# Optimization experiments

Hardware: AMD Instinct MI355X
Metric: run time of the kernel (lower is better)

Reference implementation:

```python
import jax, jax.numpy as jnp
import numpy as np

N_NODES, N_EDGES, D_FEAT, D_HID, K_CHEB = 30000, 480000, 256, 256, 2


def setup_inputs() -> dict:
    N, E, D, H, K = N_NODES, N_EDGES, D_FEAT, D_HID, K_CHEB
    key = jax.random.key(0)
    ks = jax.random.split(key, 24)
    sD = 1.0 / np.sqrt(D)
    sH = 1.0 / np.sqrt(H)
    inp = {
        "x": jax.random.normal(ks[0], (N, D), jnp.float32),
        "edge_index": jax.random.randint(ks[1], (2, E), 0, N),
        "edge_weight": jax.random.uniform(ks[2], (E,), jnp.float32),
        "h": jax.random.normal(ks[3], (N, H), jnp.float32),
        "c": jax.random.normal(ks[4], (N, H), jnp.float32),
        "src_neighbor_ids": jax.random.randint(ks[5], (E,), 0, N),
        "dst_neighbor_ids": jax.random.randint(ks[6], (E,), 0, N),
    }
    for j, nm in enumerate(["W_i", "W_f", "W_g", "W_o"]):
        inp[nm] = jax.random.normal(ks[7 + j], (D, H), jnp.float32) * sD
    for j, nm in enumerate(["Wc_i", "Wc_f", "Wc_g", "Wc_o"]):
        inp[nm] = jax.random.normal(ks[11 + j], (K, H, H), jnp.float32) * sH
    for nm in ["bc_i", "bc_f", "bc_g", "bc_o", "b_i", "b_f", "b_g", "b_o", "b_lin"]:
        inp[nm] = jnp.zeros((H,), jnp.float32)
    for j, nm in enumerate(["w_ci", "w_cf", "w_co"]):
        inp[nm] = jax.random.normal(ks[15 + j], (H,), jnp.float32) * 0.1
    inp["W_lin"] = jax.random.normal(ks[18], (H, H), jnp.float32) * sH
    return inp


def _cheb_conv(h, src, dst, norm, W, b):
    # ChebConv, K=2, sym norm, lambda_max=2: T0 = h, T1 = L_hat h = -D^-1/2 A D^-1/2 h
    out = h @ W[0]
    t1 = jax.ops.segment_sum(norm[:, None] * h[src], dst, num_segments=h.shape[0])
    return out + t1 @ W[1] + b


def reference(x, edge_index, edge_weight, h, c, src_neighbor_ids, dst_neighbor_ids,
              W_i, W_f, W_g, W_o, Wc_i, Wc_f, Wc_g, Wc_o,
              bc_i, bc_f, bc_g, bc_o, w_ci, w_cf, w_co,
              b_i, b_f, b_g, b_o, W_lin, b_lin):
    src, dst = edge_index[0], edge_index[1]
    n = x.shape[0]
    # neighbor-feature augmentation: gather both BEFORE any update, then scatter-add
    snf = x[src_neighbor_ids]
    dnf = x[dst_neighbor_ids]
    x = x.at[src].add(snf)
    x = x.at[dst].add(dnf)
    # symmetric Chebyshev normalization (lambda_max = 2 -> diagonal of L_hat is 0)
    deg = jax.ops.segment_sum(edge_weight, src, num_segments=n)
    dinv = jnp.where(deg > 0, jax.lax.rsqrt(jnp.maximum(deg, 1e-12)), 0.0)
    norm = -dinv[src] * edge_weight * dinv[dst]
    # GCLSTM gates
    i = jax.nn.sigmoid(x @ W_i + _cheb_conv(h, src, dst, norm, Wc_i, bc_i) + w_ci * c + b_i)
    f = jax.nn.sigmoid(x @ W_f + _cheb_conv(h, src, dst, norm, Wc_f, bc_f) + w_cf * c + b_f)
    g = jnp.tanh(x @ W_g + _cheb_conv(h, src, dst, norm, Wc_g, bc_g) + b_g)
    c_new = f * c + i * g
    o = jax.nn.sigmoid(x @ W_o + _cheb_conv(h, src, dst, norm, Wc_o, bc_o) + w_co * c_new + b_o)
    h0 = o * jnp.tanh(c_new)
    h_out = jax.nn.relu(h0) @ W_lin + b_lin
    return (h_out, h0, c_new)
```

## Files before the change

kernel.cpp:

```cpp
#include <hip/hip_runtime.h>
#include <math.h>

#define NN 30000
#define NE 480000
#define DH 256
#define NH (NN * DH)
#define MPAD 30080
#define CAP 48

typedef _Float16 f16x2 __attribute__((ext_vector_type(2)));
typedef _Float16 f16x4 __attribute__((ext_vector_type(4)));
typedef _Float16 f16x8 __attribute__((ext_vector_type(8)));
typedef float f32x4 __attribute__((ext_vector_type(4)));

static __device__ __forceinline__ float sigmoidf_(float x) {
    return 1.0f / (1.0f + __expf(-x));
}
static __device__ __forceinline__ float tanhf_(float x) {
    return 1.0f - 2.0f / (1.0f + __expf(2.0f * x));
}
static __device__ __forceinline__ float rsq_(float d) {
    return (d > 0.0f) ? rsqrtf(fmaxf(d, 1e-12f)) : 0.0f;
}

static __device__ __forceinline__ unsigned char f16_to_f8(_Float16 hf) {
    unsigned short b = __builtin_bit_cast(unsigned short, hf);
    unsigned s = (b >> 15) & 1u, e = (b >> 10) & 31u, m = b & 1023u;
    int ne = (int)e - 8;
    unsigned m3 = (m + 64u) >> 7;
    if (m3 == 8u) { m3 = 0u; ne += 1; }
    if (ne <= 0) return (unsigned char)(s << 7);
    if (ne > 15) ne = 15;
    return (unsigned char)((s << 7) | ((unsigned)ne << 3) | m3);
}

static __device__ __forceinline__ void f8x4_to_f32s(unsigned g, float* o) {
    unsigned m4 = g & 0x7f7f7f7fu;
    unsigned s4 = g & 0x80808080u;
#if __has_builtin(__builtin_amdgcn_perm)
    unsigned mlo = __builtin_amdgcn_perm(0u, m4, 0x04010400u);
    unsigned mhi = __builtin_amdgcn_perm(0u, m4, 0x04030402u);
    unsigned slo = __builtin_amdgcn_perm(0u, s4, 0x04010400u);
    unsigned shi = __builtin_amdgcn_perm(0u, s4, 0x04030402u);
    unsigned lo = (mlo << 7) | (slo << 8);
    unsigned hi = (mhi << 7) | (shi << 8);
#else
    unsigned lo = ((m4 & 0xffu) << 7) | ((m4 & 0xff00u) << 15)
                | ((s4 & 0xffu) << 8) | ((s4 & 0xff00u) << 16);
    unsigned hi = (((m4 >> 16) & 0xffu) << 7) | ((m4 >> 16) & 0xff00u) << 15
                | (((s4 >> 16) & 0xffu) << 8) | (((s4 >> 16) & 0xff00u) << 16);
#endif
    f16x2 vlo = __builtin_bit_cast(f16x2, lo);
    f16x2 vhi = __builtin_bit_cast(f16x2, hi);
    o[0] = (float)vlo[0]; o[1] = (float)vlo[1];
    o[2] = (float)vhi[0]; o[3] = (float)vhi[1];
}

static __device__ __forceinline__ void gload16(const _Float16* g, _Float16* l) {
    __builtin_amdgcn_global_load_lds(
        (const __attribute__((address_space(1))) void*)g,
        (__attribute__((address_space(3))) void*)l, 16, 0, 0);
}


__global__ void deg_kernel(const int* __restrict__ src, const float* __restrict__ ew,
                           float* __restrict__ deg) {
    int e = blockIdx.x * blockDim.x + threadIdx.x;
    if (e < NE) atomicAdd(&deg[src[e]], ew[e]);
}


__global__ void mega1(const int* __restrict__ src, const int* __restrict__ dst,
                      const int* __restrict__ snf, const int* __restrict__ dnf,
                      const float* __restrict__ ew,
                      int* __restrict__ cntS, int* __restrict__ cntD,
                      int* __restrict__ slotS, int2* __restrict__ slotD,
                      const float* __restrict__ x, _Float16* __restrict__ x16,
                      const float* __restrict__ h, _Float16* __restrict__ h16,
                      unsigned char* __restrict__ h8,
                      const float* __restrict__ W_i, const float* __restrict__ W_f,
                      const float* __restrict__ W_g, const float* __restrict__ W_o,
                      const float* __restrict__ Wc_i, const float* __restrict__ Wc_f,
                      const float* __restrict__ Wc_g, const float* __restrict__ Wc_o,
                      const float* __restrict__ W_lin,
                      const float* __restrict__ bc_i, const float* __restrict__ bc_f,
                      const float* __restrict__ bc_g, const float* __restrict__ bc_o,
                      const float* __restrict__ b_i, const float* __restrict__ b_f,
                      const float* __restrict__ b_g, const float* __restrict__ b_o,
                      const float* __restrict__ w_ci, const float* __restrict__ w_cf,
                      const float* __restrict__ w_co,
                      _Float16* __restrict__ WcatT, _Float16* __restrict__ WlinT,
                      float4* __restrict__ bias4, float4* __restrict__ wc4) {
    int b = blockIdx.x;
    if (b < 1875) {
        int e = b * 256 + threadIdx.x;
        int s = src[e], d = dst[e];
        int pS = atomicAdd(&cntS[s], 1);
        if (pS < CAP) slotS[s * CAP + pS] = snf[e];
        int pD = atomicAdd(&cntD[d], 1);
        if (pD < CAP) slotD[d * CAP + pD] = make_int2(s | (dnf[e] << 15),
                                                      __float_as_int(ew[e]));
        return;
    }
    b -= 1875;
    if (b < 7500) {
        int i = b * 256 + threadIdx.x;
        const int n8 = NN * 32;
        const float* in; _Float16* out; int idx; bool isH;
        if (i < n8) { in = x; out = x16; idx = i; isH = false; }
        else { in = h; out = h16; idx = i - n8; isH = true; }
        const float4 p = *reinterpret_cast<const float4*>(&in[(size_t)idx * 8]);
        const float4 q = *reinterpret_cast<const float4*>(&in[(size_t)idx * 8 + 4]);
        f16x8 v;
        v[0] = (_Float16)p.x; v[1] = (_Float16)p.y; v[2] = (_Float16)p.z; v[3] = (_Float16)p.w;
        v[4] = (_Float16)q.x; v[5] = (_Float16)q.y; v[6] = (_Float16)q.z; v[7] = (_Float16)q.w;
        *reinterpret_cast<f16x8*>(&out[(size_t)idx * 8]) = v;
        if (isH) {
            unsigned long long pk = 0;
            #pragma unroll
            for (int t = 0; t < 8; ++t)
                pk |= (unsigned long long)f16_to_f8(v[t]) << (8 * t);
            *reinterpret_cast<unsigned long long*>(&h8[(size_t)idx * 8]) = pk;
        }
        return;
    }
    b -= 7500;
    int idx = b * 256 + threadIdx.x;
    if (idx < 768 * 1024) {
        int k = idx >> 10, n = idx & 1023;
        int seg = k >> 8, kk = k & 255, nn = n >> 2, gate = n & 3;
        const float* p;
        if (seg == 0) {
            p = (gate == 0) ? W_i : (gate == 1) ? W_f : (gate == 2) ? W_g : W_o;
        } else {
            const float* base = (gate == 0) ? Wc_i : (gate == 1) ? Wc_f : (gate == 2) ? Wc_g : Wc_o;
            p = base + (seg - 1) * 65536;
        }
        WcatT[(size_t)n * 768 + k] = (_Float16)p[kk * 256 + nn];
    } else if (idx < 768 * 1024 + 256 * 256) {
        int i2 = idx - 768 * 1024;
        int k = i2 >> 8, n = i2 & 255;
        WlinT[(size_t)n * 256 + k] = (_Float16)W_lin[k * 256 + n];
    } else if (idx < 768 * 1024 + 256 * 256 + 256) {
        int f = idx - (768 * 1024 + 256 * 256);
        bias4[f] = make_float4(bc_i[f] + b_i[f], bc_f[f] + b_f[f],
                               bc_g[f] + b_g[f], bc_o[f] + b_o[f]);
        wc4[f] = make_float4(w_ci[f], w_cf[f], w_co[f], 0.f);
    }
}


__global__ __launch_bounds__(256) void fused_gather(const _Float16* __restrict__ x16,
                                                    const _Float16* __restrict__ h16,
                                                    const unsigned char* __restrict__ h8,
                                                    const int* __restrict__ cntS,
                                                    const int* __restrict__ cntD,
                                                    const int4* __restrict__ slotS4,
                                                    const int4* __restrict__ slotD4,
                                                    const float* __restrict__ deg,
                                                    _Float16* __restrict__ A16) {
    int wid = (blockIdx.x * blockDim.x + threadIdx.x) >> 6;
    int l = threadIdx.x & 63;
    if (wid >= MPAD) return;
    size_t rb = (size_t)wid * 768;
    if (wid >= NN) {
        f16x4 z = {};
        *reinterpret_cast<f16x4*>(&A16[rb + l * 4]) = z;
        *reinterpret_cast<f16x4*>(&A16[rb + 256 + l * 4]) = z;
        *reinterpret_cast<f16x4*>(&A16[rb + 512 + l * 4]) = z;
        return;
    }
    int nS = min(cntS[wid], CAP);
    int nD = min(cntD[wid], CAP);
    float dv256 = rsq_(deg[wid]) * 256.0f;

    f16x4 xv = *reinterpret_cast<const f16x4*>(&x16[(size_t)wid * 256 + l * 4]);
    f16x4 hrow = *reinterpret_cast<const f16x4*>(&h16[(size_t)wid * 256 + l * 4]);
    float a0 = (float)xv[0], a1 = (float)xv[1], a2 = (float)xv[2], a3 = (float)xv[3];
    float t0 = 0.f, t1 = 0.f, t2 = 0.f, t3 = 0.f;

    const int4* pS = &slotS4[(size_t)wid * (CAP / 4)];
    for (int j = 0; j < nS; j += 4) {
        int4 e = pS[j >> 2];
        f16x4 v0, v1, v2, v3;
        v0 = *reinterpret_cast<const f16x4*>(&x16[(size_t)e.x * 256 + l * 4]);
        if (j + 1 < nS) v1 = *reinterpret_cast<const f16x4*>(&x16[(size_t)e.y * 256 + l * 4]);
        if (j + 2 < nS) v2 = *reinterpret_cast<const f16x4*>(&x16[(size_t)e.z * 256 + l * 4]);
        if (j + 3 < nS) v3 = *reinterpret_cast<const f16x4*>(&x16[(size_t)e.w * 256 + l * 4]);
        a0 += (float)v0[0]; a1 += (float)v0[1]; a2 += (float)v0[2]; a3 += (float)v0[3];
        if (j + 1 < nS) { a0 += (float)v1[0]; a1 += (float)v1[1]; a2 += (float)v1[2]; a3 += (float)v1[3]; }
        if (j + 2 < nS) { a0 += (float)v2[0]; a1 += (float)v2[1]; a2 += (float)v2[2]; a3 += (float)v2[3]; }
        if (j + 3 < nS) { a0 += (float)v3[0]; a1 += (float)v3[1]; a2 += (float)v3[2]; a3 += (float)v3[3]; }
    }

    const int4* pD = &slotD4[(size_t)wid * (CAP / 2)];
    for (int j = 0; j < nD; j += 4) {
        int4 ea = pD[(j >> 2) * 2];
        int4 eb = pD[(j >> 2) * 2 + 1];
        int p0 = ea.x, p1 = ea.z, p2 = eb.x, p3 = eb.z;
        int s0 = p0 & 0x7fff, s1 = p1 & 0x7fff, s2 = p2 & 0x7fff, s3 = p3 & 0x7fff;
        float w0 = __int_as_float(ea.y), w1 = __int_as_float(ea.w);
        float w2 = __int_as_float(eb.y), w3 = __int_as_float(eb.w);
        f16x4 x0, x1, x2, x3;
        unsigned g0 = 0, g1 = 0, g2 = 0, g3 = 0;
        float dg0 = 0.f, dg1 = 0.f, dg2 = 0.f, dg3 = 0.f;
        x0 = *reinterpret_cast<const f16x4*>(&x16[(size_t)(p0 >> 15) * 256 + l * 4]);
        g0 = *reinterpret_cast<const unsigned*>(&h8[(size_t)s0 * 256 + l * 4]);
        dg0 = deg[s0];
        if (j + 1 < nD) {
            x1 = *reinterpret_cast<const f16x4*>(&x16[(size_t)(p1 >> 15) * 256 + l * 4]);
            g1 = *reinterpret_cast<const unsigned*>(&h8[(size_t)s1 * 256 + l * 4]);
            dg1 = deg[s1];
        }
        if (j + 2 < nD) {
            x2 = *reinterpret_cast<const f16x4*>(&x16[(size_t)(p2 >> 15) * 256 + l * 4]);
            g2 = *reinterpret_cast<const unsigned*>(&h8[(size_t)s2 * 256 + l * 4]);
            dg2 = deg[s2];
        }
        if (j + 3 < nD) {
            x3 = *reinterpret_cast<const f16x4*>(&x16[(size_t)(p3 >> 15) * 256 + l * 4]);
            g3 = *reinterpret_cast<const unsigned*>(&h8[(size_t)s3 * 256 + l * 4]);
            dg3 = deg[s3];
        }
        float n0 = -rsq_(dg0) * w0 * dv256;
        float n1 = -rsq_(dg1) * w1 * dv256;
        float n2 = -rsq_(dg2) * w2 * dv256;
        float n3 = -rsq_(dg3) * w3 * dv256;
        float hv[4];
        a0 += (float)x0[0]; a1 += (float)x0[1]; a2 += (float)x0[2]; a3 += (float)x0[3];
        f8x4_to_f32s(g0, hv);
        t0 += n0 * hv[0]; t1 += n0 * hv[1]; t2 += n0 * hv[2]; t3 += n0 * hv[3];
        if (j + 1 < nD) {
            a0 += (float)x1[0]; a1 += (float)x1[1]; a2 += (float)x1[2]; a3 += (float)x1[3];
            f8x4_to_f32s(g1, hv);
            t0 += n1 * hv[0]; t1 += n1 * hv[1]; t2 += n1 * hv[2]; t3 += n1 * hv[3];
        }
        if (j + 2 < nD) {
            a0 += (float)x2[0]; a1 += (float)x2[1]; a2 += (float)x2[2]; a3 += (float)x2[3];
            f8x4_to_f32s(g2, hv);
            t0 += n2 * hv[0]; t1 += n2 * hv[1]; t2 += n2 * hv[2]; t3 += n2 * hv[3];
        }
        if (j + 3 < nD) {
            a0 += (float)x3[0]; a1 += (float)x3[1]; a2 += (float)x3[2]; a3 += (float)x3[3];
            f8x4_to_f32s(g3, hv);
            t0 += n3 * hv[0]; t1 += n3 * hv[1]; t2 += n3 * hv[2]; t3 += n3 * hv[3];
        }
    }

    f16x4 oX, oT;
    oX[0] = (_Float16)a0; oX[1] = (_Float16)a1; oX[2] = (_Float16)a2; oX[3] = (_Float16)a3;
    oT[0] = (_Float16)t0; oT[1] = (_Float16)t1; oT[2] = (_Float16)t2; oT[3] = (_Float16)t3;
    *reinterpret_cast<f16x4*>(&A16[rb + l * 4]) = oX;
    *reinterpret_cast<f16x4*>(&A16[rb + 256 + l * 4]) = hrow;
    *reinterpret_cast<f16x4*>(&A16[rb + 512 + l * 4]) = oT;
}


#define STAGE(AS, BS, KT)                                                          \
    {                                                                              \
        _Pragma("unroll")                                                          \
        for (int i2_ = 0; i2_ < 4; ++i2_) {                                        \
            gload16(gA0 + (KT) + (size_t)i2_ * 32 * K, &AS[i2_ * 2048 + w * 512]); \
            gload16(gB0 + (KT) + (size_t)i2_ * 32 * K, &BS[i2_ * 2048 + w * 512]); \
        }                                                                          \
    }

#define COMPUTE(AS, BS)                                                            \
    {                                                                              \
        f16x8 af_[4][2], bf_[4][2];                                                \
        _Pragma("unroll")                                                          \
        for (int m_ = 0; m_ < 4; ++m_) {                                           \
            int row_ = wy * 64 + m_ * 16 + (l & 15);                               \
            _Pragma("unroll")                                                      \
            for (int ks_ = 0; ks_ < 2; ++ks_) {                                    \
                int ch_ = (ks_ * 4 + (l >> 4)) ^ (l & 7);                          \
                af_[m_][ks_] = *reinterpret_cast<const f16x8*>(&AS[row_ * 64 + ch_ * 8]); \
            }                                                                      \
        }                                                                          \
        _Pragma("unroll")                                                          \
        for (int n_ = 0; n_ < 4; ++n_) {                                           \
            int row_ = wx * 64 + n_ * 16 + (l & 15);                               \
            _Pragma("unroll")                                                      \
            for (int ks_ = 0; ks_ < 2; ++ks_) {                                    \
                int ch_ = (ks_ * 4 + (l >> 4)) ^ (l & 7);                          \
                bf_[n_][ks_] = *reinterpret_cast<const f16x8*>(&BS[row_ * 64 + ch_ * 8]); \
            }                                                                      \
        }                                                                          \
        _Pragma("unroll")                                                          \
        for (int ks_ = 0; ks_ < 2; ++ks_)                                          \
            _Pragma("unroll")                                                      \
            for (int m_ = 0; m_ < 4; ++m_)                                         \
                _Pragma("unroll")                                                  \
                for (int n_ = 0; n_ < 4; ++n_)                                     \
                    acc[m_][n_] = __builtin_amdgcn_mfma_f32_16x16x32_f16(          \
                        af_[m_][ks_], bf_[n_][ks_], acc[m_][n_], 0, 0, 0);         \
    }

template <int K, int N, bool HALF_OUT, bool DBUF>
__global__ __launch_bounds__(256) void gemm16(const _Float16* __restrict__ A,
                                              const _Float16* __restrict__ B,
                                              const float* __restrict__ bias,
                                              _Float16* __restrict__ outH,
                                              float* __restrict__ outF) {
    int tid = threadIdx.x;
    int w = tid >> 6, l = tid & 63;
    int wy = w >> 1, wx = w & 1;
    constexpr int NT = N / 128;
    constexpr int TOT = (MPAD / 128) * NT;
    constexpr int Q = TOT / 8, R = TOT & 7;
    int b = blockIdx.x;
    int xcd = b & 7, i = b >> 3;
    int v = (xcd < R ? xcd * (Q + 1) : R * (Q + 1) + (xcd - R) * Q) + i;
    int bm = (v / NT) * 128, bn = (v % NT) * 128;

    f32x4 acc[4][4];
    #pragma unroll
    for (int m = 0; m < 4; ++m)
        #pragma unroll
        for (int n = 0; n < 4; ++n)
            acc[m][n] = (f32x4){0.f, 0.f, 0.f, 0.f};

    int rowi = tid >> 3;
    int g = (tid & 7) ^ (rowi & 7);
    const _Float16* gA0 = A + (size_t)(bm + rowi) * K + g * 8;
    const _Float16* gB0 = B + (size_t)(bn + rowi) * K + g * 8;

    if constexpr (DBUF) {
        static_assert(K % 128 == 0, "counted-vmcnt dbuf needs an even K-step count");
        __shared__ _Float16 As0[8192];
        __shared__ _Float16 Bs0[8192];
        __shared__ _Float16 As1[8192];
        __shared__ _Float16 Bs1[8192];
        STAGE(As0, Bs0, 0);
        #pragma unroll
        for (int kt0 = 0; kt0 < K; kt0 += 128) {
            if (kt0 + 64 < K) {
                STAGE(As1, Bs1, kt0 + 64);
                asm volatile("s_waitcnt vmcnt(8)" ::: "memory");
            } else {
                asm volatile("s_waitcnt vmcnt(0)" ::: "memory");
            }
            asm volatile("s_barrier" ::: "memory");
            COMPUTE(As0, Bs0);
            asm volatile("s_barrier" ::: "memory");
            if (kt0 + 128 < K) {
                STAGE(As0, Bs0, kt0 + 128);
                asm volatile("s_waitcnt vmcnt(8)" ::: "memory");
            } else {
                asm volatile("s_waitcnt vmcnt(0)" ::: "memory");
            }
            asm volatile("s_barrier" ::: "memory");
            COMPUTE(As1, Bs1);
            asm volatile("s_barrier" ::: "memory");
        }
    } else {
        __shared__ _Float16 As[8192];
        __shared__ _Float16 Bs[8192];
        for (int kt = 0; kt < K; kt += 64) {
            STAGE(As, Bs, kt);
            __syncthreads();
            COMPUTE(As, Bs);
            __syncthreads();
        }
    }

    #pragma unroll
    for (int m = 0; m < 4; ++m) {
        #pragma unroll
        for (int n = 0; n < 4; ++n) {
            int col = bn + wx * 64 + n * 16 + (l & 15);
            #pragma unroll
            for (int j = 0; j < 4; ++j) {
                int row = bm + wy * 64 + m * 16 + (l >> 4) * 4 + j;
                if (row < NN) {
                    if constexpr (HALF_OUT)
                        outH[(size_t)row * N + col] = (_Float16)acc[m][n][j];
                    else
                        outF[(size_t)row * N + col] = acc[m][n][j] + bias[col];
                }
            }
        }
    }
}


__global__ void gate_kernel(const _Float16* __restrict__ pre, const float* __restrict__ c,
                            const float4* __restrict__ bias4, const float4* __restrict__ wc4,
                            float* __restrict__ h0p, float* __restrict__ cnp,
                            _Float16* __restrict__ relu16) {
    int idx = blockIdx.x * blockDim.x + threadIdx.x;
    if (idx >= MPAD * 128) return;
    int row = idx >> 7, f0 = (idx & 127) << 1;
    size_t o = (size_t)row * 256 + f0;
    if (row >= NN) {
        *reinterpret_cast<f16x2*>(&relu16[o]) = (f16x2){(_Float16)0.f, (_Float16)0.f};
        return;
    }
    f16x8 pv = *reinterpret_cast<const f16x8*>(&pre[(size_t)row * 1024 + f0 * 4]);
    float2 cv = *reinterpret_cast<const float2*>(&c[o]);
    float4 b4a = bias4[f0], b4b = bias4[f0 + 1];
    float4 w4a = wc4[f0], w4b = wc4[f0 + 1];
    float iv0 = sigmoidf_((float)pv[0] + b4a.x + w4a.x * cv.x);
    float fv0 = sigmoidf_((float)pv[1] + b4a.y + w4a.y * cv.x);
    float gv0 = tanhf_((float)pv[2] + b4a.z);
    float cn0 = fv0 * cv.x + iv0 * gv0;
    float ov0 = sigmoidf_((float)pv[3] + b4a.w + w4a.z * cn0);
    float h00 = ov0 * tanhf_(cn0);
    float iv1 = sigmoidf_((float)pv[4] + b4b.x + w4b.x * cv.y);
    float fv1 = sigmoidf_((float)pv[5] + b4b.y + w4b.y * cv.y);
    float gv1 = tanhf_((float)pv[6] + b4b.z);
    float cn1 = fv1 * cv.y + iv1 * gv1;
    float ov1 = sigmoidf_((float)pv[7] + b4b.w + w4b.z * cn1);
    float h01 = ov1 * tanhf_(cn1);
    *reinterpret_cast<float2*>(&cnp[o]) = make_float2(cn0, cn1);
    *reinterpret_cast<float2*>(&h0p[o]) = make_float2(h00, h01);
    *reinterpret_cast<f16x2*>(&relu16[o]) =
        (f16x2){(_Float16)fmaxf(h00, 0.f), (_Float16)fmaxf(h01, 0.f)};
}


extern "C" void kernel_launch(void* const* d_in, const int* in_sizes, int n_in,
                              void* d_out, int out_size, void* d_ws, size_t ws_size,
                              hipStream_t stream) {
    const float* x   = (const float*)d_in[0];
    const int*   ei  = (const int*)d_in[1];
    const float* ew  = (const float*)d_in[2];
    const float* h   = (const float*)d_in[3];
    const float* c   = (const float*)d_in[4];
    const int*   snf = (const int*)d_in[5];
    const int*   dnf = (const int*)d_in[6];
    const float* W_i = (const float*)d_in[7];
    const float* W_f = (const float*)d_in[8];
    const float* W_g = (const float*)d_in[9];
    const float* W_o = (const float*)d_in[10];
    const float* Wc_i = (const float*)d_in[11];
    const float* Wc_f = (const float*)d_in[12];
    const float* Wc_g = (const float*)d_in[13];
    const float* Wc_o = (const float*)d_in[14];
    const float* bc_i = (const float*)d_in[15];
    const float* bc_f = (const float*)d_in[16];
    const float* bc_g = (const float*)d_in[17];
    const float* bc_o = (const float*)d_in[18];
    const float* b_i  = (const float*)d_in[19];
    const float* b_f  = (const float*)d_in[20];
    const float* b_g  = (const float*)d_in[21];
    const float* b_o  = (const float*)d_in[22];
    const float* b_lin = (const float*)d_in[23];
    const float* w_ci = (const float*)d_in[24];
    const float* w_cf = (const float*)d_in[25];
    const float* w_co = (const float*)d_in[26];
    const float* W_lin = (const float*)d_in[27];

    const int* src = ei;
    const int* dst = ei + NE;

    float* out = (float*)d_out;
    float* houtp = out;
    float* h0p   = out + NH;
    float* cnp   = out + 2 * NH;

    char* ws = (char*)d_ws;
    _Float16* pre16 = (_Float16*)ws;
    int* cntS = (int*)ws;
    int* cntD = (int*)(ws + 131072);
    float* deg = (float*)(ws + 262144);
    int* slotS = (int*)(ws + 393216);
    int2* slotD = (int2*)(ws + 6153216);
    _Float16* h16 = (_Float16*)(ws + 17673216);
    unsigned char* h8 = (unsigned char*)(ws + 33033216);

    _Float16* A16 = (_Float16*)(ws + 61440000);
    _Float16* relu16 = A16;
    _Float16* WcatT = (_Float16*)(ws + 107642880);
    _Float16* WlinT = (_Float16*)(ws + 109215744);
    float4* bias4 = (float4*)(ws + 109346816);
    float4* wc4 = (float4*)(ws + 109350912);
    _Float16* x16 = (_Float16*)(ws + 109477888);

    hipMemsetAsync(ws, 0, 393216, stream);

    deg_kernel<<<1875, 256, 0, stream>>>(src, ew, deg);

    mega1<<<12704, 256, 0, stream>>>(src, dst, snf, dnf, ew,
                                     cntS, cntD, slotS, slotD,
                                     x, x16, h, h16, h8,
                                     W_i, W_f, W_g, W_o, Wc_i, Wc_f, Wc_g, Wc_o, W_lin,
                                     bc_i, bc_f, bc_g, bc_o, b_i, b_f, b_g, b_o,
                                     w_ci, w_cf, w_co,
                                     WcatT, WlinT, bias4, wc4);

    fused_gather<<<7520, 256, 0, stream>>>(x16, h16, h8, cntS, cntD,
                                           (const int4*)slotS, (const int4*)slotD,
                                           deg, A16);

    gemm16<768, 1024, true, true><<<1880, 256, 0, stream>>>(A16, WcatT, nullptr, pre16, nullptr);

    gate_kernel<<<15040, 256, 0, stream>>>(pre16, c, bias4, wc4, h0p, cnp, relu16);

    gemm16<256, 256, false, false><<<470, 256, 0, stream>>>(relu16, WlinT, b_lin, nullptr, houtp);
}
```

Before: 310.1 us.

## Use 256x128 tiles with 512 threads for the gate pre-activation GEMM

```diff
diff --git a/kernel.cpp b/kernel.cpp
--- a/kernel.cpp
+++ b/kernel.cpp
@@ -6,6 +6,7 @@
 #define DH 256
 #define NH (NN * DH)
 #define MPAD 30080
+#define MPAD2 30208
 #define CAP 48
 
 typedef _Float16 f16x2 __attribute__((ext_vector_type(2)));
@@ -256,52 +257,91 @@
 }
 
 
-#define STAGE(AS, BS, KT)                                                          \
-    {                                                                              \
-        _Pragma("unroll")                                                          \
-        for (int i2_ = 0; i2_ < 4; ++i2_) {                                        \
-            gload16(gA0 + (KT) + (size_t)i2_ * 32 * K, &AS[i2_ * 2048 + w * 512]); \
-            gload16(gB0 + (KT) + (size_t)i2_ * 32 * K, &BS[i2_ * 2048 + w * 512]); \
-        }                                                                          \
-    }
-
-#define COMPUTE(AS, BS)                                                            \
-    {                                                                              \
-        f16x8 af_[4][2], bf_[4][2];                                                \
-        _Pragma("unroll")                                                          \
-        for (int m_ = 0; m_ < 4; ++m_) {                                           \
-            int row_ = wy * 64 + m_ * 16 + (l & 15);                               \
-            _Pragma("unroll")                                                      \
-            for (int ks_ = 0; ks_ < 2; ++ks_) {                                    \
-                int ch_ = (ks_ * 4 + (l >> 4)) ^ (l & 7);                          \
-                af_[m_][ks_] = *reinterpret_cast<const f16x8*>(&AS[row_ * 64 + ch_ * 8]); \
-            }                                                                      \
-        }                                                                          \
-        _Pragma("unroll")                                                          \
-        for (int n_ = 0; n_ < 4; ++n_) {                                           \
-            int row_ = wx * 64 + n_ * 16 + (l & 15);                               \
-            _Pragma("unroll")                                                      \
-            for (int ks_ = 0; ks_ < 2; ++ks_) {                                    \
-                int ch_ = (ks_ * 4 + (l >> 4)) ^ (l & 7);                          \
-                bf_[n_][ks_] = *reinterpret_cast<const f16x8*>(&BS[row_ * 64 + ch_ * 8]); \
-            }                                                                      \
-        }                                                                          \
-        _Pragma("unroll")                                                          \
-        for (int ks_ = 0; ks_ < 2; ++ks_)                                          \
-            _Pragma("unroll")                                                      \
-            for (int m_ = 0; m_ < 4; ++m_)                                         \
-                _Pragma("unroll")                                                  \
-                for (int n_ = 0; n_ < 4; ++n_)                                     \
-                    acc[m_][n_] = __builtin_amdgcn_mfma_f32_16x16x32_f16(          \
-                        af_[m_][ks_], bf_[n_][ks_], acc[m_][n_], 0, 0, 0);         \
-    }
-
-template <int K, int N, bool HALF_OUT, bool DBUF>
-__global__ __launch_bounds__(256) void gemm16(const _Float16* __restrict__ A,
-                                              const _Float16* __restrict__ B,
-                                              const float* __restrict__ bias,
-                                              _Float16* __restrict__ outH,
-                                              float* __restrict__ outF) {
+__global__ __launch_bounds__(512) void gemm_pre8(const _Float16* __restrict__ A,
+                                                 const _Float16* __restrict__ B,
+                                                 _Float16* __restrict__ outH) {
+    constexpr int K = 768, N = 1024;
+    __shared__ _Float16 As[256 * 64];
+    __shared__ _Float16 Bs[128 * 64];
+    int tid = threadIdx.x;
+    int w = tid >> 6, l = tid & 63;
+    int wr = w >> 1, wc = w & 1;
+    constexpr int NT = N / 128;
+    constexpr int TOT = (MPAD2 / 256) * NT;
+    constexpr int Q = TOT / 8;
+    int b = blockIdx.x;
+    int v = (b & 7) * Q + (b >> 3);
+    int bm = (v / NT) * 256, bn = (v % NT) * 128;
+
+    f32x4 acc[4][4];
+    #pragma unroll
+    for (int m = 0; m < 4; ++m)
+        #pragma unroll
+        for (int n = 0; n < 4; ++n)
+            acc[m][n] = (f32x4){0.f, 0.f, 0.f, 0.f};
+
+    int rowi = tid >> 3;
+    int g = (tid & 7) ^ (rowi & 7);
+    const _Float16* gA0 = A + (size_t)(bm + rowi) * K + g * 8;
+    const _Float16* gB0 = B + (size_t)(bn + rowi) * K + g * 8;
+
+    for (int kt = 0; kt < K; kt += 64) {
+        #pragma unroll
+        for (int i2 = 0; i2 < 4; ++i2)
+            gload16(gA0 + kt + (size_t)i2 * 64 * K, &As[i2 * 4096 + w * 512]);
+        #pragma unroll
+        for (int i2 = 0; i2 < 2; ++i2)
+            gload16(gB0 + kt + (size_t)i2 * 64 * K, &Bs[i2 * 4096 + w * 512]);
+        __syncthreads();
+
+        #pragma unroll
+        for (int ks = 0; ks < 2; ++ks) {
+            f16x8 af[4], bf[4];
+            #pragma unroll
+            for (int m = 0; m < 4; ++m) {
+                int row = wr * 64 + m * 16 + (l & 15);
+                int ch = (ks * 4 + (l >> 4)) ^ (l & 7);
+                af[m] = *reinterpret_cast<const f16x8*>(&As[row * 64 + ch * 8]);
+            }
+            #pragma unroll
+            for (int n = 0; n < 4; ++n) {
+                int row = wc * 64 + n * 16 + (l & 15);
+                int ch = (ks * 4 + (l >> 4)) ^ (l & 7);
+                bf[n] = *reinterpret_cast<const f16x8*>(&Bs[row * 64 + ch * 8]);
+            }
+            #pragma unroll
+            for (int m = 0; m < 4; ++m)
+                #pragma unroll
+                for (int n = 0; n < 4; ++n)
+                    acc[m][n] = __builtin_amdgcn_mfma_f32_16x16x32_f16(
+                        af[m], bf[n], acc[m][n], 0, 0, 0);
+        }
+        __syncthreads();
+    }
+
+    #pragma unroll
+    for (int m = 0; m < 4; ++m) {
+        #pragma unroll
+        for (int n = 0; n < 4; ++n) {
+            int col = bn + wc * 64 + n * 16 + (l & 15);
+            #pragma unroll
+            for (int j = 0; j < 4; ++j) {
+                int row = bm + wr * 64 + m * 16 + (l >> 4) * 4 + j;
+                if (row < NN)
+                    outH[(size_t)row * N + col] = (_Float16)acc[m][n][j];
+            }
+        }
+    }
+}
+
+
+__global__ __launch_bounds__(256) void gemm_lin_k(const _Float16* __restrict__ A,
+                                                  const _Float16* __restrict__ B,
+                                                  const float* __restrict__ bias,
+                                                  float* __restrict__ outF) {
+    constexpr int K = 256, N = 256;
+    __shared__ _Float16 As[8192];
+    __shared__ _Float16 Bs[8192];
     int tid = threadIdx.x;
     int w = tid >> 6, l = tid & 63;
     int wy = w >> 1, wx = w & 1;
@@ -325,43 +365,36 @@
     const _Float16* gA0 = A + (size_t)(bm + rowi) * K + g * 8;
     const _Float16* gB0 = B + (size_t)(bn + rowi) * K + g * 8;
 
-    if constexpr (DBUF) {
-        static_assert(K % 128 == 0, "counted-vmcnt dbuf needs an even K-step count");
-        __shared__ _Float16 As0[8192];
-        __shared__ _Float16 Bs0[8192];
-        __shared__ _Float16 As1[8192];
-        __shared__ _Float16 Bs1[8192];
-        STAGE(As0, Bs0, 0);
-        #pragma unroll
-        for (int kt0 = 0; kt0 < K; kt0 += 128) {
-            if (kt0 + 64 < K) {
-                STAGE(As1, Bs1, kt0 + 64);
-                asm volatile("s_waitcnt vmcnt(8)" ::: "memory");
-            } else {
-                asm volatile("s_waitcnt vmcnt(0)" ::: "memory");
+    for (int kt = 0; kt < K; kt += 64) {
+        #pragma unroll
+        for (int i2 = 0; i2 < 4; ++i2) {
+            gload16(gA0 + kt + (size_t)i2 * 32 * K, &As[i2 * 2048 + w * 512]);
+            gload16(gB0 + kt + (size_t)i2 * 32 * K, &Bs[i2 * 2048 + w * 512]);
+        }
+        __syncthreads();
+        #pragma unroll
+        for (int ks = 0; ks < 2; ++ks) {
+            f16x8 af[4], bf[4];
+            #pragma unroll
+            for (int m = 0; m < 4; ++m) {
+                int row = wy * 64 + m * 16 + (l & 15);
+                int ch = (ks * 4 + (l >> 4)) ^ (l & 7);
+                af[m] = *reinterpret_cast<const f16x8*>(&As[row * 64 + ch * 8]);
             }
-            asm volatile("s_barrier" ::: "memory");
-            COMPUTE(As0, Bs0);
-            asm volatile("s_barrier" ::: "memory");
-            if (kt0 + 128 < K) {
-                STAGE(As0, Bs0, kt0 + 128);
-                asm volatile("s_waitcnt vmcnt(8)" ::: "memory");
-            } else {
-                asm volatile("s_waitcnt vmcnt(0)" ::: "memory");
+            #pragma unroll
+            for (int n = 0; n < 4; ++n) {
+                int row = wx * 64 + n * 16 + (l & 15);
+                int ch = (ks * 4 + (l >> 4)) ^ (l & 7);
+                bf[n] = *reinterpret_cast<const f16x8*>(&Bs[row * 64 + ch * 8]);
             }
-            asm volatile("s_barrier" ::: "memory");
-            COMPUTE(As1, Bs1);
-            asm volatile("s_barrier" ::: "memory");
-        }
-    } else {
-        __shared__ _Float16 As[8192];
-        __shared__ _Float16 Bs[8192];
-        for (int kt = 0; kt < K; kt += 64) {
-            STAGE(As, Bs, kt);
-            __syncthreads();
-            COMPUTE(As, Bs);
-            __syncthreads();
-        }
+            #pragma unroll
+            for (int m = 0; m < 4; ++m)
+                #pragma unroll
+                for (int n = 0; n < 4; ++n)
+                    acc[m][n] = __builtin_amdgcn_mfma_f32_16x16x32_f16(
+                        af[m], bf[n], acc[m][n], 0, 0, 0);
+        }
+        __syncthreads();
     }
 
     #pragma unroll
@@ -372,12 +405,8 @@
             #pragma unroll
             for (int j = 0; j < 4; ++j) {
                 int row = bm + wy * 64 + m * 16 + (l >> 4) * 4 + j;
-                if (row < NN) {
-                    if constexpr (HALF_OUT)
-                        outH[(size_t)row * N + col] = (_Float16)acc[m][n][j];
-                    else
-                        outF[(size_t)row * N + col] = acc[m][n][j] + bias[col];
-                }
+                if (row < NN)
+                    outF[(size_t)row * N + col] = acc[m][n][j] + bias[col];
             }
         }
     }
@@ -471,11 +500,11 @@
 
     _Float16* A16 = (_Float16*)(ws + 61440000);
     _Float16* relu16 = A16;
-    _Float16* WcatT = (_Float16*)(ws + 107642880);
-    _Float16* WlinT = (_Float16*)(ws + 109215744);
-    float4* bias4 = (float4*)(ws + 109346816);
-    float4* wc4 = (float4*)(ws + 109350912);
-    _Float16* x16 = (_Float16*)(ws + 109477888);
+    _Float16* WcatT = (_Float16*)(ws + 107839488);
+    _Float16* WlinT = (_Float16*)(ws + 109412352);
+    float4* bias4 = (float4*)(ws + 109543424);
+    float4* wc4 = (float4*)(ws + 109547520);
+    _Float16* x16 = (_Float16*)(ws + 109551616);
 
     hipMemsetAsync(ws, 0, 393216, stream);
 
@@ -493,9 +522,9 @@
                                            (const int4*)slotS, (const int4*)slotD,
                                            deg, A16);
 
-    gemm16<768, 1024, true, true><<<1880, 256, 0, stream>>>(A16, WcatT, nullptr, pre16, nullptr);
+    gemm_pre8<<<944, 512, 0, stream>>>(A16, WcatT, pre16);
 
     gate_kernel<<<15040, 256, 0, stream>>>(pre16, c, bias4, wc4, h0p, cnp, relu16);
 
-    gemm16<256, 256, false, false><<<470, 256, 0, stream>>>(relu16, WlinT, b_lin, nullptr, houtp);
-}
+    gemm_lin_k<<<470, 256, 0, stream>>>(relu16, WlinT, b_lin, houtp);
+}
```

Result: no change. 310.4 us (+0.1%).
